# Performance work log

Measured on AMD Instinct MI355X. Metric: run time of the kernel, lower is better.

Reference implementation:

```python
import jax, jax.numpy as jnp
import numpy as np

T, F, C, V, H, E, S = 256, 32, 8, 10000, 1024, 256, 512
PAD, BOS, EOS = 0, 1, 2


def setup_inputs() -> dict:
    key = jax.random.key(0)
    ks = jax.random.split(key, 16)
    sH = 1.0 / np.sqrt(H).astype(np.float32)
    inp = {
        'token_ctx': jax.random.normal(ks[0], (1, S, H), jnp.float32),
        'char_emb_w': jax.random.normal(ks[1], (V, E), jnp.float32) * 0.02,
        'enc_W_ih': jax.random.normal(ks[2], (3 * H, E), jnp.float32) * sH,
        'enc_W_hh': jax.random.normal(ks[3], (3 * H, H), jnp.float32) * sH,
        'enc_b_ih': jnp.zeros((3 * H,), jnp.float32),
        'enc_b_hh': jnp.zeros((3 * H,), jnp.float32),
        'dec_W_ih': jax.random.normal(ks[4], (3 * H, E), jnp.float32) * sH,
        'dec_W_hh': jax.random.normal(ks[5], (3 * H, H), jnp.float32) * sH,
        'dec_b_ih': jnp.zeros((3 * H,), jnp.float32),
        'dec_b_hh': jnp.zeros((3 * H,), jnp.float32),
        'out_W': jax.random.normal(ks[6], (V, H), jnp.float32) * sH,
        'out_b': jnp.zeros((V,), jnp.float32),
    }
    # (token_id, xtoken_idx, char_id) triples; every token 1..T has exactly C chars
    tok_ids = jnp.repeat(jnp.arange(1, T + 1, dtype=jnp.int32), C)
    xt_ids = jax.random.randint(ks[7], (T * C,), 0, S, jnp.int32)
    ch_ids = jax.random.randint(ks[8], (T * C,), 4, V, jnp.int32)  # avoid specials
    inp['in_sent_token_chars'] = jnp.stack([tok_ids, xt_ids, ch_ids], axis=-1)[None]
    gold = jax.random.randint(ks[9], (T * F,), 4, V, jnp.int32)  # no EOS -> full-length decode
    inp['out_chars'] = jnp.concatenate([jnp.array([BOS], jnp.int32), gold])[None]
    inp['max_tokens'] = T
    inp['max_form_len'] = F
    inp['use_teacher_forcing'] = 1
    return inp


def _gru_cell(x, h, W_ih, W_hh, b_ih, b_hh):
    # PyTorch GRU cell convention; x:[T,E], h:[T,H]
    gi = x @ W_ih.T + b_ih
    gh = h @ W_hh.T + b_hh
    i_r, i_z, i_n = jnp.split(gi, 3, axis=-1)
    h_r, h_z, h_n = jnp.split(gh, 3, axis=-1)
    r = jax.nn.sigmoid(i_r + h_r)
    z = jax.nn.sigmoid(i_z + h_z)
    n = jnp.tanh(i_n + r * h_n)
    return (1.0 - z) * n + z * h


def reference(token_ctx, char_emb_w, enc_W_ih, enc_W_hh, enc_b_ih, enc_b_hh,
              dec_W_ih, dec_W_hh, dec_b_ih, dec_b_hh, out_W, out_b,
              in_sent_token_chars, out_chars, max_tokens, max_form_len,
              use_teacher_forcing):
    Vout = out_b.shape[0]
    # ragged mask select per token id -> here every token has exactly C chars
    tc = in_sent_token_chars[0].reshape(max_tokens, -1, 3)  # [T, C, 3]
    chars = tc[:, :, 2]          # [T, C]
    xtoken_ids = tc[:, :, 1]     # [T, C]
    # enc_state = mean over the token's xtoken contexts
    h0 = jnp.mean(token_ctx[0][xtoken_ids], axis=1)  # [T, H]
    # ---- encoder GRU over the token's chars (batched over tokens) ----
    x_enc = char_emb_w[chars]  # [T, C, E]

    def enc_step(h, x):
        return _gru_cell(x, h, enc_W_ih, enc_W_hh, enc_b_ih, enc_b_hh), None

    h_enc, _ = jax.lax.scan(enc_step, h0, jnp.swapaxes(x_enc, 0, 1))  # [T, H]
    # ---- decoder GRU, max_form_len steps, teacher-forced, EOS freeze+pad ----
    # gold char for token t at step s is out_chars[0, t*F + s + 1]
    gold = out_chars[0, 1:1 + max_tokens * max_form_len].reshape(max_tokens, max_form_len)
    c0 = jnp.full((max_tokens,), out_chars[0, 0], dtype=out_chars.dtype)
    done0 = (c0 == EOS)
    last0 = jnp.zeros((max_tokens, Vout), jnp.float32)

    def dec_step(carry, g):
        h, c, done, last = carry
        x = char_emb_w[c]
        h_new = _gru_cell(x, h, dec_W_ih, dec_W_hh, dec_b_ih, dec_b_hh)
        s_new = h_new @ out_W.T + out_b
        score = jnp.where(done[:, None], last, s_new)  # pad with last score after EOS
        h = jnp.where(done[:, None], h, h_new)         # state frozen after EOS
        if use_teacher_forcing:
            c_next = g
        else:
            c_next = jnp.argmax(s_new, axis=-1).astype(c.dtype)
        done = done | (c_next == EOS)
        return (h, c_next, done, score), score

    _, scores = jax.lax.scan(dec_step, (h_enc, c0, done0, last0),
                             jnp.swapaxes(gold, 0, 1))  # [F, T, V]
    # torch.cat(dec_scores, dim=1): token-major, step-minor -> [1, T*F, V]
    return jnp.transpose(scores, (1, 0, 2)).reshape(1, max_tokens * max_form_len, Vout)
```

## Files before the change

### kernel.cpp

```cpp
#include <hip/hip_runtime.h>
#include <hip/hip_bf16.h>
#include <math.h>

#define TT   256
#define FF   32
#define CCH  8
#define VV   10000
#define HH   1024
#define EE   256
#define NG   3072
#define EOS_ID 2
#define NSTEPS 40
#define CHAIN_BLKS 256
#define CTR_INTS 512

#define LDS_GP_OFF    98304
#define LDS_STB_OFF   (98304 + 53248)
#define LDS_TOTAL     (98304 + 53248 + 2048)

typedef __attribute__((ext_vector_type(8))) short bf16x8;
typedef __attribute__((ext_vector_type(4))) float f32x4;

__device__ __forceinline__ void gload_lds16(const void* g, void* l) {
    __builtin_amdgcn_global_load_lds((const __attribute__((address_space(1))) void*)g,
                                     (__attribute__((address_space(3))) void*)l,
                                     16, 0, 0);
}

__device__ __forceinline__ float sigmf(float x) { return 1.f / (1.f + __expf(-x)); }

__global__ __launch_bounds__(256) void prep_kernel(const int* __restrict__ oc,
                                                   int* __restrict__ c_in,
                                                   unsigned char* __restrict__ done,
                                                   int* __restrict__ ctr) {
    int t = threadIdx.x;
    for (int i = t; i < CTR_INTS; i += 256) ctr[i] = 0;
    int c0 = oc[0];
    bool d = (c0 == EOS_ID);
    for (int f = 0; f < FF; ++f) {
        c_in[t * FF + f] = (f == 0) ? c0 : oc[1 + t * FF + f - 1];
        done[t * FF + f] = d ? 1 : 0;
        d = d || (oc[1 + t * FF + f] == EOS_ID);
    }
}

__global__ __launch_bounds__(256) void h0_kernel(const float* __restrict__ tctx,
                                                 const int* __restrict__ sent,
                                                 float* __restrict__ h,
                                                 __hip_bfloat16* __restrict__ A0) {
    int t = blockIdx.x;
    int tid = threadIdx.x;
    __shared__ int xt[CCH];
    if (tid < CCH) xt[tid] = sent[(t * CCH + tid) * 3 + 1];
    __syncthreads();
#pragma unroll
    for (int jj = 0; jj < 4; ++jj) {
        int j = tid + jj * 256;
        float s = 0.f;
#pragma unroll
        for (int c = 0; c < CCH; ++c) s += tctx[(size_t)xt[c] * HH + j];
        float hv = s * 0.125f;
        h[(size_t)t * HH + j] = hv;
        A0[(size_t)t * HH + j] = __float2bfloat16(hv);
    }
}

__global__ __launch_bounds__(256) void f2b_kernel(const float* __restrict__ src,
                                                  __hip_bfloat16* __restrict__ dst) {
    size_t base = ((size_t)blockIdx.x * 256 + threadIdx.x) * 4;
    float4 v = *(const float4*)(src + base);
    dst[base + 0] = __float2bfloat16(v.x);
    dst[base + 1] = __float2bfloat16(v.y);
    dst[base + 2] = __float2bfloat16(v.z);
    dst[base + 3] = __float2bfloat16(v.w);
}

__global__ __launch_bounds__(256) void build_Bg2(const float* __restrict__ Whh,
                                                 __hip_bfloat16* __restrict__ Bg) {
    int by = blockIdx.x;
    int tid = threadIdx.x;
    int jb = by / 48, rr = by % 48;
    int g = rr >> 4, jj = rr & 15;
    const float* srow = Whh + (size_t)(g * 1024 + jb * 16 + jj) * HH;
    __hip_bfloat16* drow = Bg + (size_t)by * HH;
    float4 v = *(const float4*)(srow + tid * 4);
    drow[tid * 4 + 0] = __float2bfloat16(v.x);
    drow[tid * 4 + 1] = __float2bfloat16(v.y);
    drow[tid * 4 + 2] = __float2bfloat16(v.z);
    drow[tid * 4 + 3] = __float2bfloat16(v.w);
}

template<int MODE>
__global__ __launch_bounds__(256) void gemm_pipe(const __hip_bfloat16* __restrict__ A, int lda,
                                                 const __hip_bfloat16* __restrict__ B, int ldb,
                                                 __hip_bfloat16* __restrict__ Cb,
                                                 const int* __restrict__ idsrc,
                                                 int NIT) {
    __shared__ __hip_bfloat16 As[4][128 * 32];
    __shared__ __hip_bfloat16 Bs[4][128 * 32];
    __shared__ int sids[128];

    const int tid = threadIdx.x;
    const int n0 = blockIdx.x * 128;
    const int m0 = blockIdx.y * 128;

    if (tid < 128) {
        int row = m0 + tid;
        int t = row & 255;
        int id;
        if (MODE == 1) { int c = row >> 8; id = idsrc[(t * CCH + c) * 3 + 2]; }
        else           { int f = row >> 8; id = idsrc[t * FF + f]; }
        sids[tid] = id;
    }
    __syncthreads();

    const int srow = tid >> 2, skq = tid & 3;
    const int l = tid & 63;
    const int w = tid >> 6;
    const int wr = (w >> 1) * 64, wc = (w & 1) * 64;
    const int fra = ((wr + (l & 15)) << 5) + ((l >> 4) << 3);
    const int frb = ((wc + (l & 15)) << 5) + ((l >> 4) << 3);

    f32x4 acc[4][4];
#pragma unroll
    for (int i = 0; i < 4; ++i)
#pragma unroll
        for (int j = 0; j < 4; ++j) acc[i][j] = (f32x4){0.f, 0.f, 0.f, 0.f};

    auto stage = [&](int slot, int it) {
        const int k0 = it * 32;
        const __hip_bfloat16* ga0 = A + (size_t)sids[srow] * lda + k0 + skq * 8;
        const __hip_bfloat16* ga1 = A + (size_t)sids[64 + srow] * lda + k0 + skq * 8;
        const __hip_bfloat16* gb0 = B + (size_t)(n0 + srow) * ldb + k0 + skq * 8;
        const __hip_bfloat16* gb1 = B + (size_t)(n0 + 64 + srow) * ldb + k0 + skq * 8;
        __hip_bfloat16* lA = &As[slot][tid * 8];
        __hip_bfloat16* lB = &Bs[slot][tid * 8];
        gload_lds16(ga0, lA);
        gload_lds16(ga1, lA + 2048);
        gload_lds16(gb0, lB);
        gload_lds16(gb1, lB + 2048);
    };

    stage(0, 0);
    stage(1, 1);

    for (int it = 0; it < NIT; ++it) {
        if (it + 2 < NIT) stage((it + 2) & 3, it + 2);
        int ahead = NIT - 1 - it; if (ahead > 2) ahead = 2;
        if (ahead >= 2)      asm volatile("s_waitcnt vmcnt(8)" ::: "memory");
        else if (ahead == 1) asm volatile("s_waitcnt vmcnt(4)" ::: "memory");
        else                 asm volatile("s_waitcnt vmcnt(0)" ::: "memory");
        __builtin_amdgcn_s_barrier();
        __builtin_amdgcn_sched_barrier(0);

        const __hip_bfloat16* cA = As[it & 3];
        const __hip_bfloat16* cB = Bs[it & 3];
        bf16x8 af[4], bfv[4];
#pragma unroll
        for (int fm = 0; fm < 4; ++fm) af[fm] = *(const bf16x8*)&cA[fra + fm * 512];
#pragma unroll
        for (int fn = 0; fn < 4; ++fn) bfv[fn] = *(const bf16x8*)&cB[frb + fn * 512];
#pragma unroll
        for (int fm = 0; fm < 4; ++fm)
#pragma unroll
            for (int fn = 0; fn < 4; ++fn)
                acc[fm][fn] = __builtin_amdgcn_mfma_f32_16x16x32_bf16(af[fm], bfv[fn], acc[fm][fn], 0, 0, 0);
    }

    const int colb = wc + (l & 15);
    const int rb   = wr + ((l >> 4) << 2);
#pragma unroll
    for (int fm = 0; fm < 4; ++fm)
#pragma unroll
        for (int fn = 0; fn < 4; ++fn)
#pragma unroll
            for (int q = 0; q < 4; ++q)
                Cb[(size_t)(m0 + rb + fm * 16 + q) * NG + n0 + colb + fn * 16] =
                    __float2bfloat16(acc[fm][fn][q]);
}

__global__ __launch_bounds__(256, 1) void chain_kernel(
    __hip_bfloat16* Abuf0, __hip_bfloat16* Abuf1,
    const __hip_bfloat16* __restrict__ Bg_e,
    const __hip_bfloat16* __restrict__ Bg_d,
    const __hip_bfloat16* __restrict__ gi_enc, const __hip_bfloat16* __restrict__ gi_dec,
    const float* __restrict__ ebih, const float* __restrict__ ebhh,
    const float* __restrict__ dbih, const float* __restrict__ dbhh,
    const float* __restrict__ hA,
    __hip_bfloat16* __restrict__ hsb,
    const unsigned char* __restrict__ dflags,
    int* flags) {

    extern __shared__ __align__(16) char smem[];
    char* Bs = smem;
    float* gp = (float*)(smem + LDS_GP_OFF);
    __hip_bfloat16* stb = (__hip_bfloat16*)(smem + LDS_STB_OFF);

    const int tid = threadIdx.x;
    const int b = blockIdx.x;
    const int mt = b >> 6, jb = b & 63;
    const int m0 = mt * 64;
    const int jbase = jb * 16;

    const int l = tid & 63, w = tid >> 6;
    const int ji = tid & 15;
    const int rg = tid >> 4;
    const int j = jbase + ji;
    const int lrow = l & 15;
    const int lk8  = (l >> 4) << 3;

    float hreg[4];
#pragma unroll
    for (int p = 0; p < 4; ++p)
        hreg[p] = hA[(size_t)(m0 + p * 16 + rg) * HH + j];

    const float e_br = ebih[j] + ebhh[j];
    const float e_bz = ebih[HH + j] + ebhh[HH + j];
    const float e_bi = ebih[2 * HH + j];
    const float e_bh = ebhh[2 * HH + j];
    const float d_br = dbih[j] + dbhh[j];
    const float d_bz = dbih[HH + j] + dbhh[HH + j];
    const float d_bi = dbih[2 * HH + j];
    const float d_bh = dbhh[2 * HH + j];

    auto stageBfull = [&](const __hip_bfloat16* Bp) {
#pragma unroll
        for (int c = 0; c < 24; ++c) {
            int chunk = c * 256 + tid;
            int row = chunk >> 7, q = chunk & 127;
            const char* src = (const char*)(Bp + (size_t)row * HH) + ((q ^ (row & 7)) << 4);
            gload_lds16(src, Bs + chunk * 16);
        }
    };

    auto ldB = [&](int nt, int ks) -> bf16x8 {
        int r = nt * 16 + lrow;
        int g = ks * 4 + (l >> 4);
        return *(const bf16x8*)(Bs + r * 2048 + ((g ^ (r & 7)) << 4));
    };

    unsigned int gru[4], gzu[4], gnu[4];
    int dfl[4] = {0, 0, 0, 0};
#pragma unroll
    for (int p = 0; p < 4; ++p) {
        const __hip_bfloat16* gb = gi_enc + (size_t)(m0 + p * 16 + rg) * NG + j;
        asm volatile("global_load_ushort %0, %1, off nt" : "=v"(gru[p]) : "v"(gb));
        asm volatile("global_load_ushort %0, %1, off nt" : "=v"(gzu[p]) : "v"(gb + HH));
        asm volatile("global_load_ushort %0, %1, off nt" : "=v"(gnu[p]) : "v"(gb + 2 * HH));
    }

    for (int s = 0; s < NSTEPS; ++s) {
        if (s > 0) {
            if (tid < 64) {
                const int* fp = flags + (mt << 6) + l;
                long guard = 0;
                for (;;) {
                    int v;
                    asm volatile("global_load_dword %0, %1, off sc0 sc1" : "=v"(v) : "v"(fp));
                    asm volatile("s_waitcnt vmcnt(0)" ::: "memory");
                    if (__all(v >= s)) break;
                    if (++guard > (1L << 22)) break;
                    __builtin_amdgcn_s_sleep(2);
                }
            }
            __syncthreads();
        }

        if (s == 0 || s == CCH) {
            stageBfull(((s == 0) ? Bg_e : Bg_d) + (size_t)jb * 48 * HH);
            asm volatile("s_waitcnt vmcnt(0)" ::: "memory");
            __syncthreads();
        }

        const __hip_bfloat16* Ab = (s & 1) ? Abuf1 : Abuf0;
        __hip_bfloat16* An = (s & 1) ? Abuf0 : Abuf1;

        asm volatile("s_waitcnt vmcnt(0)" ::: "memory");
        const __hip_bfloat16* ap0 = Ab + (size_t)(m0 + 0 * 16 + lrow) * HH + w * 256 + lk8;
        const __hip_bfloat16* ap1 = Ab + (size_t)(m0 + 1 * 16 + lrow) * HH + w * 256 + lk8;
        const __hip_bfloat16* ap2 = Ab + (size_t)(m0 + 2 * 16 + lrow) * HH + w * 256 + lk8;
        const __hip_bfloat16* ap3 = Ab + (size_t)(m0 + 3 * 16 + lrow) * HH + w * 256 + lk8;

        bf16x8 av[8][4];
#pragma unroll
        for (int ksl = 0; ksl < 8; ++ksl) {
            asm volatile("global_load_dwordx4 %0, %1, off sc0 sc1" : "=v"(av[ksl][0]) : "v"(ap0 + ksl * 32));
            asm volatile("global_load_dwordx4 %0, %1, off sc0 sc1" : "=v"(av[ksl][1]) : "v"(ap1 + ksl * 32));
            asm volatile("global_load_dwordx4 %0, %1, off sc0 sc1" : "=v"(av[ksl][2]) : "v"(ap2 + ksl * 32));
            asm volatile("global_load_dwordx4 %0, %1, off sc0 sc1" : "=v"(av[ksl][3]) : "v"(ap3 + ksl * 32));
        }

        f32x4 acc[4][3];
#pragma unroll
        for (int m = 0; m < 4; ++m)
#pragma unroll
            for (int nt = 0; nt < 3; ++nt) acc[m][nt] = (f32x4){0.f, 0.f, 0.f, 0.f};

        const int kbase = w * 8;
        bf16x8 bb[3][3];
#pragma unroll
        for (int nt = 0; nt < 3; ++nt) { bb[0][nt] = ldB(nt, kbase); bb[1][nt] = ldB(nt, kbase + 1); }

#pragma unroll
        for (int ksl = 0; ksl < 8; ++ksl) {
            if (ksl + 2 < 8) {
#pragma unroll
                for (int nt = 0; nt < 3; ++nt) bb[(ksl + 2) % 3][nt] = ldB(nt, kbase + ksl + 2);
            }
            asm volatile("s_waitcnt vmcnt(%0)" :: "i"(28 - 4 * ksl) : "memory");
            __builtin_amdgcn_sched_barrier(0);
#pragma unroll
            for (int m = 0; m < 4; ++m)
#pragma unroll
                for (int nt = 0; nt < 3; ++nt)
                    acc[m][nt] = __builtin_amdgcn_mfma_f32_16x16x32_bf16(av[ksl][m], bb[ksl % 3][nt], acc[m][nt], 0, 0, 0);
        }

        {
            float* gpw = gp + w * (64 * 52);
            const int rbase = (l >> 4) << 2;
#pragma unroll
            for (int m = 0; m < 4; ++m)
#pragma unroll
                for (int nt = 0; nt < 3; ++nt)
#pragma unroll
                    for (int q = 0; q < 4; ++q)
                        gpw[(m * 16 + rbase + q) * 52 + nt * 16 + lrow] = acc[m][nt][q];
        }
        __syncthreads();

        const int f = s - CCH;
        const float br_ = (s < CCH) ? e_br : d_br;
        const float bz_ = (s < CCH) ? e_bz : d_bz;
        const float bi_ = (s < CCH) ? e_bi : d_bi;
        const float bh_ = (s < CCH) ? e_bh : d_bh;
#pragma unroll
        for (int p = 0; p < 4; ++p) {
            const int tr = p * 16 + rg;
            float racc = 0.f, zacc = 0.f, nacc = 0.f;
#pragma unroll
            for (int ww = 0; ww < 4; ++ww) {
                const float* g = gp + ww * (64 * 52) + tr * 52;
                racc += g[ji];
                zacc += g[16 + ji];
                nacc += g[32 + ji];
            }
            float grf = __uint_as_float(gru[p] << 16);
            float gzf = __uint_as_float(gzu[p] << 16);
            float gnf = __uint_as_float(gnu[p] << 16);
            float r = sigmf(grf + br_ + racc);
            float z = sigmf(gzf + bz_ + zacc);
            float n = tanhf(gnf + bi_ + r * (nacc + bh_));
            float hold = hreg[p];
            float hv = (1.f - z) * n + z * hold;
            if (s >= CCH && dfl[p]) hv = hold;
            hreg[p] = hv;
            stb[tr * 16 + ji] = __float2bfloat16(hv);
        }
        __syncthreads();

        if (s < NSTEPS - 1) {
            if (tid < 128) {
                const int row = tid >> 1, part = tid & 1;
                bf16x8 v = *(const bf16x8*)&stb[row * 16 + part * 8];
                const __hip_bfloat16* ap = An + (size_t)(m0 + row) * HH + jbase + part * 8;
                asm volatile("global_store_dwordx4 %0, %1, off sc0 sc1"
                             :: "v"(ap), "v"(v) : "memory");
            }
            asm volatile("s_waitcnt vmcnt(0)" ::: "memory");
            __syncthreads();
            if (tid == 0) {
                int v = s + 1;
                int* fp = flags + (mt << 6) + jb;
                asm volatile("global_store_dword %0, %1, off sc0 sc1"
                             :: "v"(fp), "v"(v) : "memory");
            }
        }
        if (s >= CCH && tid < 128) {
            const int row = tid >> 1, part = tid & 1;
            bf16x8 v = *(const bf16x8*)&stb[row * 16 + part * 8];
            bf16x8* hp = (bf16x8*)(hsb + ((size_t)f * TT + m0 + row) * HH + jbase + part * 8);
            __builtin_nontemporal_store(v, hp);
        }
        if (s < NSTEPS - 1) {
            const __hip_bfloat16* gnext = (s + 1 < CCH) ? (gi_enc + (size_t)(s + 1) * TT * NG)
                                                        : (gi_dec + (size_t)(s + 1 - CCH) * TT * NG);
#pragma unroll
            for (int p = 0; p < 4; ++p) {
                const __hip_bfloat16* gb = gnext + (size_t)(m0 + p * 16 + rg) * NG + j;
                asm volatile("global_load_ushort %0, %1, off nt" : "=v"(gru[p]) : "v"(gb));
                asm volatile("global_load_ushort %0, %1, off nt" : "=v"(gzu[p]) : "v"(gb + HH));
                asm volatile("global_load_ushort %0, %1, off nt" : "=v"(gnu[p]) : "v"(gb + 2 * HH));
            }
            if (s + 1 >= CCH) {
                const int fnx = s + 1 - CCH;
#pragma unroll
                for (int p = 0; p < 4; ++p) {
                    const unsigned char* dp = dflags + (size_t)(m0 + p * 16 + rg) * FF + fnx;
                    asm volatile("global_load_ubyte %0, %1, off" : "=v"(dfl[p]) : "v"(dp));
                }
            }
        }
    }
}

__global__ __launch_bounds__(256) void scores_pipe(const __hip_bfloat16* __restrict__ hsb,
                                                   const __hip_bfloat16* __restrict__ Wb,
                                                   const float* __restrict__ bout,
                                                   const int* __restrict__ oc,
                                                   float* __restrict__ out) {
    __shared__ __hip_bfloat16 As[4][128 * 32];
    __shared__ __hip_bfloat16 Bs[4][128 * 32];
    int bid = blockIdx.x;
    int sid = (bid & 7) * 632 + (bid >> 3);
    int bx = sid % 79, by = sid / 79;
    int n0 = bx * 128, m0 = by * 128;

    const int tid = threadIdx.x;
    const int l = tid & 63;
    const int w = tid >> 6;
    const int wr = (w >> 1) * 64, wc = (w & 1) * 64;
    const int srow = tid >> 2, skq = tid & 3;

    f32x4 acc[4][4];
#pragma unroll
    for (int i = 0; i < 4; ++i)
#pragma unroll
        for (int j = 0; j < 4; ++j) acc[i][j] = (f32x4){0.f, 0.f, 0.f, 0.f};

    int br0 = n0 + srow, br1 = n0 + 64 + srow;
    br0 = (br0 > VV - 1) ? VV - 1 : br0;
    br1 = (br1 > VV - 1) ? VV - 1 : br1;
    const __hip_bfloat16* gA0 = hsb + (size_t)(m0 + srow) * HH + skq * 8;
    const __hip_bfloat16* gA1 = hsb + (size_t)(m0 + 64 + srow) * HH + skq * 8;
    const __hip_bfloat16* gB0 = Wb + (size_t)br0 * HH + skq * 8;
    const __hip_bfloat16* gB1 = Wb + (size_t)br1 * HH + skq * 8;
    const int fra = ((wr + (l & 15)) << 5) + ((l >> 4) << 3);
    const int frb = ((wc + (l & 15)) << 5) + ((l >> 4) << 3);

    auto stage = [&](int slot, int it) {
        const int k0 = it * 32;
        __hip_bfloat16* lA = &As[slot][tid * 8];
        __hip_bfloat16* lB = &Bs[slot][tid * 8];
        gload_lds16(gA0 + k0, lA);
        gload_lds16(gA1 + k0, lA + 2048);
        gload_lds16(gB0 + k0, lB);
        gload_lds16(gB1 + k0, lB + 2048);
    };

    stage(0, 0);
    stage(1, 1);

    for (int it = 0; it < 32; ++it) {
        if (it + 2 < 32) stage((it + 2) & 3, it + 2);
        int ahead = 31 - it; if (ahead > 2) ahead = 2;
        if (ahead >= 2)      asm volatile("s_waitcnt vmcnt(8)" ::: "memory");
        else if (ahead == 1) asm volatile("s_waitcnt vmcnt(4)" ::: "memory");
        else                 asm volatile("s_waitcnt vmcnt(0)" ::: "memory");
        __builtin_amdgcn_s_barrier();
        __builtin_amdgcn_sched_barrier(0);

        const __hip_bfloat16* cA = As[it & 3];
        const __hip_bfloat16* cB = Bs[it & 3];
        bf16x8 af[4], bfv[4];
#pragma unroll
        for (int fm = 0; fm < 4; ++fm) af[fm] = *(const bf16x8*)&cA[fra + fm * 512];
#pragma unroll
        for (int fn = 0; fn < 4; ++fn) bfv[fn] = *(const bf16x8*)&cB[frb + fn * 512];
#pragma unroll
        for (int fm = 0; fm < 4; ++fm)
#pragma unroll
            for (int fn = 0; fn < 4; ++fn)
                acc[fm][fn] = __builtin_amdgcn_mfma_f32_16x16x32_bf16(af[fm], bfv[fn], acc[fm][fn], 0, 0, 0);
    }

    const bool zf = (oc[0] == EOS_ID);
    const int colb = wc + (l & 15);
    const int rb   = wr + ((l >> 4) << 2);
#pragma unroll
    for (int fn = 0; fn < 4; ++fn) {
        int v = n0 + colb + fn * 16;
        if (v < VV) {
            float bb = bout[v];
#pragma unroll
            for (int fm = 0; fm < 4; ++fm) {
#pragma unroll
                for (int q = 0; q < 4; ++q) {
                    int m = m0 + rb + fm * 16 + q;
                    int fo = m >> 8, t = m & 255;
                    float val = zf ? 0.f : (acc[fm][fn][q] + bb);
                    __builtin_nontemporal_store(val, &out[(size_t)(t * FF + fo) * VV + v]);
                }
            }
        }
    }
}

extern "C" void kernel_launch(void* const* d_in, const int* in_sizes, int n_in,
                              void* d_out, int out_size, void* d_ws, size_t ws_size,
                              hipStream_t stream) {
    (void)in_sizes; (void)n_in; (void)ws_size;

    const float* token_ctx = (const float*)d_in[0];
    const float* emb       = (const float*)d_in[1];
    const float* eWih      = (const float*)d_in[2];
    const float* eWhh      = (const float*)d_in[3];
    const float* ebih      = (const float*)d_in[4];
    const float* ebhh      = (const float*)d_in[5];
    const float* dWih      = (const float*)d_in[6];
    const float* dWhh      = (const float*)d_in[7];
    const float* dbih      = (const float*)d_in[8];
    const float* dbhh      = (const float*)d_in[9];
    const float* Wout      = (const float*)d_in[10];
    const float* bout      = (const float*)d_in[11];
    const int*   sent      = (const int*)d_in[12];
    const int*   ochars    = (const int*)d_in[13];
    float* out = (float*)d_out;

    char* w = (char*)d_ws;
    float* hA = (float*)w;                      w += (size_t)TT * HH * 4;
    __hip_bfloat16* Ab0 = (__hip_bfloat16*)w;   w += (size_t)TT * HH * 2;
    __hip_bfloat16* Ab1 = (__hip_bfloat16*)w;   w += (size_t)TT * HH * 2;
    __hip_bfloat16* hsb = (__hip_bfloat16*)w;   w += (size_t)FF * TT * HH * 2;
    __hip_bfloat16* Woutb = (__hip_bfloat16*)w; w += (size_t)VV * HH * 2;
    int* c_in = (int*)w;                        w += (size_t)TT * FF * 4;
    unsigned char* done = (unsigned char*)w;    w += (size_t)TT * FF;
    w = (char*)(((size_t)w + 255) & ~(size_t)255);
    int* ctr = (int*)w;                         w += (size_t)CTR_INTS * 4;

    char* tail = (char*)d_out + (size_t)out_size * 4;
    tail -= (size_t)NG * HH * 2;          __hip_bfloat16* Bg_e = (__hip_bfloat16*)tail;
    tail -= (size_t)NG * HH * 2;          __hip_bfloat16* Bg_d = (__hip_bfloat16*)tail;
    tail -= (size_t)CCH * TT * NG * 2;    __hip_bfloat16* gi_enc = (__hip_bfloat16*)tail;
    tail -= (size_t)FF * TT * NG * 2;     __hip_bfloat16* gi_dec = (__hip_bfloat16*)tail;
    tail -= (size_t)VV * EE * 2;          __hip_bfloat16* emb_bf = (__hip_bfloat16*)tail;
    tail -= (size_t)NG * EE * 2;          __hip_bfloat16* Wihb_e = (__hip_bfloat16*)tail;
    tail -= (size_t)NG * EE * 2;          __hip_bfloat16* Wihb_d = (__hip_bfloat16*)tail;

    hipFuncSetAttribute((const void*)chain_kernel,
                        hipFuncAttributeMaxDynamicSharedMemorySize, LDS_TOTAL);

    prep_kernel<<<1, 256, 0, stream>>>(ochars, c_in, done, ctr);
    h0_kernel<<<TT, 256, 0, stream>>>(token_ctx, sent, hA, Ab0);
    f2b_kernel<<<(VV * EE) / 4 / 256, 256, 0, stream>>>(emb, emb_bf);
    f2b_kernel<<<(NG * EE) / 4 / 256, 256, 0, stream>>>(eWih, Wihb_e);
    f2b_kernel<<<(NG * EE) / 4 / 256, 256, 0, stream>>>(dWih, Wihb_d);
    f2b_kernel<<<(VV * HH) / 4 / 256, 256, 0, stream>>>(Wout, Woutb);
    build_Bg2<<<NG, 256, 0, stream>>>(eWhh, Bg_e);
    build_Bg2<<<NG, 256, 0, stream>>>(dWhh, Bg_d);

    gemm_pipe<1><<<dim3(24, 16), 256, 0, stream>>>(emb_bf, EE, Wihb_e, EE, gi_enc, sent, 8);
    gemm_pipe<2><<<dim3(24, 64), 256, 0, stream>>>(emb_bf, EE, Wihb_d, EE, gi_dec, c_in, 8);

    chain_kernel<<<CHAIN_BLKS, 256, LDS_TOTAL, stream>>>(Ab0, Ab1, Bg_e, Bg_d,
                                                         gi_enc, gi_dec,
                                                         ebih, ebhh, dbih, dbhh,
                                                         hA, hsb, done, ctr);

    scores_pipe<<<5056, 256, 0, stream>>>(hsb, Woutb, bout, ochars, out);
}
```

Measured before the change: 693.5 us.

## Enlarge output-projection GEMM tile to 256x256 with swizzled LDS layout

Result: faster. 627.8 us (-9.5%).

```diff
diff --git a/kernel.cpp b/kernel.cpp
--- a/kernel.cpp
+++ b/kernel.cpp
@@ -17,6 +17,8 @@
 #define LDS_GP_OFF    98304
 #define LDS_STB_OFF   (98304 + 53248)
 #define LDS_TOTAL     (98304 + 53248 + 2048)
+
+#define SC_LDS_TOTAL  131072
 
 typedef __attribute__((ext_vector_type(8))) short bf16x8;
 typedef __attribute__((ext_vector_type(4))) float f32x4;
@@ -404,48 +406,52 @@
     }
 }
 
-__global__ __launch_bounds__(256) void scores_pipe(const __hip_bfloat16* __restrict__ hsb,
-                                                   const __hip_bfloat16* __restrict__ Wb,
-                                                   const float* __restrict__ bout,
-                                                   const int* __restrict__ oc,
-                                                   float* __restrict__ out) {
-    __shared__ __hip_bfloat16 As[4][128 * 32];
-    __shared__ __hip_bfloat16 Bs[4][128 * 32];
-    int bid = blockIdx.x;
-    int sid = (bid & 7) * 632 + (bid >> 3);
-    int bx = sid % 79, by = sid / 79;
-    int n0 = bx * 128, m0 = by * 128;
+__global__ __launch_bounds__(512, 2) void scores256(const __hip_bfloat16* __restrict__ hsb,
+                                                    const __hip_bfloat16* __restrict__ Wb,
+                                                    const float* __restrict__ bout,
+                                                    const int* __restrict__ oc,
+                                                    float* __restrict__ out) {
+    extern __shared__ __align__(16) char smem[];
+
+    const int bid = blockIdx.x;
+    const int sid = (bid & 7) * 160 + (bid >> 3);
+    const int bx = sid % 40, by = sid / 40;
+    const int n0 = bx * 256, m0 = by * 256;
 
     const int tid = threadIdx.x;
     const int l = tid & 63;
     const int w = tid >> 6;
-    const int wr = (w >> 1) * 64, wc = (w & 1) * 64;
-    const int srow = tid >> 2, skq = tid & 3;
-
-    f32x4 acc[4][4];
-#pragma unroll
-    for (int i = 0; i < 4; ++i)
+    const int wm = w >> 2;
+    const int wn = w & 3;
+    const int lrow = l & 15;
+    const int qg = l >> 4;
+
+    f32x4 acc[8][4];
+#pragma unroll
+    for (int i = 0; i < 8; ++i)
 #pragma unroll
         for (int j = 0; j < 4; ++j) acc[i][j] = (f32x4){0.f, 0.f, 0.f, 0.f};
-
-    int br0 = n0 + srow, br1 = n0 + 64 + srow;
-    br0 = (br0 > VV - 1) ? VV - 1 : br0;
-    br1 = (br1 > VV - 1) ? VV - 1 : br1;
-    const __hip_bfloat16* gA0 = hsb + (size_t)(m0 + srow) * HH + skq * 8;
-    const __hip_bfloat16* gA1 = hsb + (size_t)(m0 + 64 + srow) * HH + skq * 8;
-    const __hip_bfloat16* gB0 = Wb + (size_t)br0 * HH + skq * 8;
-    const __hip_bfloat16* gB1 = Wb + (size_t)br1 * HH + skq * 8;
-    const int fra = ((wr + (l & 15)) << 5) + ((l >> 4) << 3);
-    const int frb = ((wc + (l & 15)) << 5) + ((l >> 4) << 3);
 
     auto stage = [&](int slot, int it) {
         const int k0 = it * 32;
-        __hip_bfloat16* lA = &As[slot][tid * 8];
-        __hip_bfloat16* lB = &Bs[slot][tid * 8];
-        gload_lds16(gA0 + k0, lA);
-        gload_lds16(gA1 + k0, lA + 2048);
-        gload_lds16(gB0 + k0, lB);
-        gload_lds16(gB1 + k0, lB + 2048);
+        char* sb = smem + slot * 32768;
+#pragma unroll
+        for (int cc = 0; cc < 2; ++cc) {
+            int chunk = cc * 512 + tid;
+            int row = chunk >> 2, q = chunk & 3;
+            int qsrc = q ^ (((row >> 1) & 3) ^ (row & 1));
+            const __hip_bfloat16* src = hsb + (size_t)(m0 + row) * HH + k0 + qsrc * 8;
+            gload_lds16(src, sb + chunk * 16);
+        }
+#pragma unroll
+        for (int cc = 0; cc < 2; ++cc) {
+            int chunk = cc * 512 + tid;
+            int row = chunk >> 2, q = chunk & 3;
+            int br = n0 + row; if (br > VV - 1) br = VV - 1;
+            int qsrc = q ^ (((row >> 1) & 3) ^ (row & 1));
+            const __hip_bfloat16* src = Wb + (size_t)br * HH + k0 + qsrc * 8;
+            gload_lds16(src, sb + 16384 + chunk * 16);
+        }
     };
 
     stage(0, 0);
@@ -460,30 +466,38 @@
         __builtin_amdgcn_s_barrier();
         __builtin_amdgcn_sched_barrier(0);
 
-        const __hip_bfloat16* cA = As[it & 3];
-        const __hip_bfloat16* cB = Bs[it & 3];
-        bf16x8 af[4], bfv[4];
-#pragma unroll
-        for (int fm = 0; fm < 4; ++fm) af[fm] = *(const bf16x8*)&cA[fra + fm * 512];
-#pragma unroll
-        for (int fn = 0; fn < 4; ++fn) bfv[fn] = *(const bf16x8*)&cB[frb + fn * 512];
-#pragma unroll
-        for (int fm = 0; fm < 4; ++fm)
+        const char* cA = smem + (it & 3) * 32768;
+        const char* cB = cA + 16384;
+        bf16x8 af[8], bfv[4];
+#pragma unroll
+        for (int fm = 0; fm < 8; ++fm) {
+            int r = wm * 128 + fm * 16 + lrow;
+            int qpos = qg ^ (((r >> 1) & 3) ^ (r & 1));
+            af[fm] = *(const bf16x8*)(cA + r * 64 + qpos * 16);
+        }
+#pragma unroll
+        for (int fn = 0; fn < 4; ++fn) {
+            int r = wn * 64 + fn * 16 + lrow;
+            int qpos = qg ^ (((r >> 1) & 3) ^ (r & 1));
+            bfv[fn] = *(const bf16x8*)(cB + r * 64 + qpos * 16);
+        }
+#pragma unroll
+        for (int fm = 0; fm < 8; ++fm)
 #pragma unroll
             for (int fn = 0; fn < 4; ++fn)
                 acc[fm][fn] = __builtin_amdgcn_mfma_f32_16x16x32_bf16(af[fm], bfv[fn], acc[fm][fn], 0, 0, 0);
     }
 
     const bool zf = (oc[0] == EOS_ID);
-    const int colb = wc + (l & 15);
-    const int rb   = wr + ((l >> 4) << 2);
+    const int colb = wn * 64 + lrow;
+    const int rb   = wm * 128 + (qg << 2);
 #pragma unroll
     for (int fn = 0; fn < 4; ++fn) {
         int v = n0 + colb + fn * 16;
         if (v < VV) {
             float bb = bout[v];
 #pragma unroll
-            for (int fm = 0; fm < 4; ++fm) {
+            for (int fm = 0; fm < 8; ++fm) {
 #pragma unroll
                 for (int q = 0; q < 4; ++q) {
                     int m = m0 + rb + fm * 16 + q;
@@ -521,12 +535,12 @@
     float* hA = (float*)w;                      w += (size_t)TT * HH * 4;
     __hip_bfloat16* Ab0 = (__hip_bfloat16*)w;   w += (size_t)TT * HH * 2;
     __hip_bfloat16* Ab1 = (__hip_bfloat16*)w;   w += (size_t)TT * HH * 2;
-    __hip_bfloat16* hsb = (__hip_bfloat16*)w;   w += (size_t)FF * TT * HH * 2;
     __hip_bfloat16* Woutb = (__hip_bfloat16*)w; w += (size_t)VV * HH * 2;
     int* c_in = (int*)w;                        w += (size_t)TT * FF * 4;
     unsigned char* done = (unsigned char*)w;    w += (size_t)TT * FF;
     w = (char*)(((size_t)w + 255) & ~(size_t)255);
     int* ctr = (int*)w;                         w += (size_t)CTR_INTS * 4;
+    __hip_bfloat16* hsb = (__hip_bfloat16*)w;   w += (size_t)FF * TT * HH * 2;
 
     char* tail = (char*)d_out + (size_t)out_size * 4;
     tail -= (size_t)NG * HH * 2;          __hip_bfloat16* Bg_e = (__hip_bfloat16*)tail;
@@ -539,6 +553,8 @@
 
     hipFuncSetAttribute((const void*)chain_kernel,
                         hipFuncAttributeMaxDynamicSharedMemorySize, LDS_TOTAL);
+    hipFuncSetAttribute((const void*)scores256,
+                        hipFuncAttributeMaxDynamicSharedMemorySize, SC_LDS_TOTAL);
 
     prep_kernel<<<1, 256, 0, stream>>>(ochars, c_in, done, ctr);
     h0_kernel<<<TT, 256, 0, stream>>>(token_ctx, sent, hA, Ab0);
@@ -557,5 +573,5 @@
                                                          ebih, ebhh, dbih, dbhh,
                                                          hA, hsb, done, ctr);
 
-    scores_pipe<<<5056, 256, 0, stream>>>(hsb, Woutb, bout, ochars, out);
-}
+    scores256<<<1280, 512, SC_LDS_TOTAL, stream>>>(hsb, Woutb, bout, ochars, out);
+}
```
